# Optimization experiments

Hardware: AMD Instinct MI355X
Metric: run time of the kernel (lower is better)

Reference implementation:

```python
import jax, jax.numpy as jnp
import numpy as np

N, K, CIN, COUT = 150000, 27, 32, 64
EPS = 1e-5
NEG_SLOPE = 0.01


def setup_inputs() -> dict:
    key = jax.random.key(0)
    k1, k2, k3, k4, k5, k6 = jax.random.split(key, 6)
    feats = jax.random.normal(k1, (N, CIN), dtype=jnp.float32)
    nbr = jax.random.randint(k2, (N, K), 0, N, dtype=jnp.int32)
    mask = jax.random.randint(k3, (N, K), 0, 2, dtype=jnp.int32).astype(jnp.bool_)
    # per-offset conv weights [K, Cin, Cout], kaiming-ish scale
    W = jax.random.normal(k4, (K, CIN, COUT), dtype=jnp.float32) / np.sqrt(K * CIN)
    gamma = jax.random.normal(k5, (COUT,), dtype=jnp.float32) * 0.1 + 1.0
    beta = jax.random.normal(k6, (COUT,), dtype=jnp.float32) * 0.1
    return {"feats": feats, "W": W, "gamma": gamma, "beta": beta, "nbr": nbr, "mask": mask}


def reference(feats, W, gamma, beta, nbr, mask):
    # sparse conv as gather-GEMM-(implicit scatter): out[n] = sum_k W[k]^T f[nbr[n,k]]
    gathered = jnp.where(mask[..., None], feats[nbr], 0.0)          # [N, K, Cin]
    out = jnp.einsum('nkc,kcd->nd', gathered, W)                     # [N, Cout]
    # BatchNorm over voxel axis (training-mode batch stats)
    mean = jnp.mean(out, axis=0)
    var = jnp.var(out, axis=0)
    out = (out - mean) * jax.lax.rsqrt(var + EPS) * gamma + beta
    # LeakyReLU, negative_slope = 0.01
    return jnp.where(out >= 0, out, NEG_SLOPE * out)
```

## Files before the change

### kernel.cpp

```cpp
#include <hip/hip_runtime.h>

#define N_VOX  150000
#define KNBR   27
#define CIN    32
#define COUT   64
#define NBUCKET 64
#define NEG_SLOPE 0.01f
#define EPS 1e-5f
#define APPLY_BLOCKS 1024

typedef __bf16 bf16x8 __attribute__((ext_vector_type(8)));
typedef float  f32x4  __attribute__((ext_vector_type(4)));

#define NB_FEATS 2344
#define NB_W       27
#define NB_Z       32

__global__ __launch_bounds__(256) void prep_all(
    const float* __restrict__ feats, const float* __restrict__ W,
    __bf16* __restrict__ fb, __bf16* __restrict__ Wp,
    float* __restrict__ bsums)
{
    const int t = threadIdx.x;
    int b = blockIdx.x;

    if (b < NB_FEATS) {
        const int i = b * 256 + t;
        if (i < N_VOX * CIN / 8) {
            const float4* p = reinterpret_cast<const float4*>(feats) + (size_t)i * 2;
            const float4 a = p[0], c = p[1];
            bf16x8 o;
            o[0]=(__bf16)a.x; o[1]=(__bf16)a.y; o[2]=(__bf16)a.z; o[3]=(__bf16)a.w;
            o[4]=(__bf16)c.x; o[5]=(__bf16)c.y; o[6]=(__bf16)c.z; o[7]=(__bf16)c.w;
            reinterpret_cast<bf16x8*>(fb)[i] = o;
        }
        return;
    }
    b -= NB_FEATS;

    if (b < NB_W) {
        const int u = b * 256 + t;
        const int lane = u & 63, f = u >> 6;
        const int s = f & 3, k = f >> 2;
        const int n = lane & 15, q = lane >> 4;
        const float* src = W + ((size_t)(k * CIN + q * 8) * COUT + s * 16 + n);
        bf16x8 o;
#pragma unroll
        for (int j = 0; j < 8; ++j) o[j] = (__bf16)src[(size_t)j * COUT];
        reinterpret_cast<bf16x8*>(Wp)[u] = o;
        return;
    }
    b -= NB_W;

    const int z = b * 256 + t;
    if (z < NBUCKET * 2 * COUT) bsums[z] = 0.0f;
}

__global__ __launch_bounds__(256, 3) void conv_mfma3(
    const __bf16* __restrict__ fb,
    const __bf16* __restrict__ Wp,
    const int* __restrict__ nbr,
    const int* __restrict__ mask,
    float* __restrict__ out,
    float* __restrict__ bsums)
{
    const int t    = threadIdx.x;
    const int wave = t >> 6;
    const int lane = t & 63;
    const int n16  = lane & 15;
    const int q    = lane >> 4;
    const int arow = blockIdx.x * 64 + wave * 16 + n16;
    const bool rowok = arow < N_VOX;
    const size_t nb = (size_t)(rowok ? arow : 0) * KNBR;

    int idx[KNBR];
#pragma unroll
    for (int k = 0; k < KNBR; ++k) {
        const int m  = mask[nb + k];
        const int ix = nbr[nb + k];
        idx[k] = (rowok && m != 0) ? ix : -1;
    }

    const bf16x8* __restrict__ bp = reinterpret_cast<const bf16x8*>(Wp);
    const bf16x8 zv = {};

    f32x4 acc0 = {0.f,0.f,0.f,0.f}, acc1 = {0.f,0.f,0.f,0.f};
    f32x4 acc2 = {0.f,0.f,0.f,0.f}, acc3 = {0.f,0.f,0.f,0.f};

#pragma unroll 9
    for (int k = 0; k < KNBR; ++k) {
        const bool v  = idx[k] >= 0;
        const int  ie = v ? idx[k] : 0;
        bf16x8 a = *reinterpret_cast<const bf16x8*>(fb + (size_t)ie * CIN + q * 8);
        if (!v) a = zv;
        const bf16x8 b0 = bp[(k * 4 + 0) * 64 + lane];
        const bf16x8 b1 = bp[(k * 4 + 1) * 64 + lane];
        const bf16x8 b2 = bp[(k * 4 + 2) * 64 + lane];
        const bf16x8 b3 = bp[(k * 4 + 3) * 64 + lane];
        acc0 = __builtin_amdgcn_mfma_f32_16x16x32_bf16(a, b0, acc0, 0, 0, 0);
        acc1 = __builtin_amdgcn_mfma_f32_16x16x32_bf16(a, b1, acc1, 0, 0, 0);
        acc2 = __builtin_amdgcn_mfma_f32_16x16x32_bf16(a, b2, acc2, 0, 0, 0);
        acc3 = __builtin_amdgcn_mfma_f32_16x16x32_bf16(a, b3, acc3, 0, 0, 0);
    }

    const int orow_base = blockIdx.x * 64 + wave * 16 + q * 4;
    f32x4 accs[4] = {acc0, acc1, acc2, acc3};
#pragma unroll
    for (int r = 0; r < 4; ++r) {
        const int orow = orow_base + r;
        if (orow < N_VOX) {
            float* dst = out + (size_t)orow * COUT + n16;
#pragma unroll
            for (int s = 0; s < 4; ++s) dst[s * 16] = accs[s][r];
        }
    }

    float* dstb = bsums + ((blockIdx.x * 4 + wave) & (NBUCKET - 1)) * (2 * COUT);
#pragma unroll
    for (int s = 0; s < 4; ++s) {
        float ps = accs[s][0] + accs[s][1] + accs[s][2] + accs[s][3];
        float pq = accs[s][0] * accs[s][0] + accs[s][1] * accs[s][1]
                 + accs[s][2] * accs[s][2] + accs[s][3] * accs[s][3];
        ps += __shfl_down(ps, 32); ps += __shfl_down(ps, 16);
        pq += __shfl_down(pq, 32); pq += __shfl_down(pq, 16);
        if (q == 0) {
            atomicAdd(dstb + s * 16 + n16, ps);
            atomicAdd(dstb + COUT + s * 16 + n16, pq);
        }
    }
}

__global__ __launch_bounds__(256) void bn_stats_apply(
    float* __restrict__ out, const float* __restrict__ bsums,
    const float* __restrict__ gamma, const float* __restrict__ beta)
{
    __shared__ float s_sc[COUT], s_sh[COUT];
    const int t = threadIdx.x;
    if (t < COUT) {
        float s = 0.f, qq = 0.f;
#pragma unroll 8
        for (int b = 0; b < NBUCKET; ++b) {
            s  += bsums[b * (2 * COUT) + t];
            qq += bsums[b * (2 * COUT) + COUT + t];
        }
        const float inv_n = 1.0f / (float)N_VOX;
        const float mean  = s * inv_n;
        const float var   = qq * inv_n - mean * mean;
        const float scale = gamma[t] * rsqrtf(var + EPS);
        s_sc[t] = scale;
        s_sh[t] = beta[t] - mean * scale;
    }
    __syncthreads();

    const long total4 = (long)N_VOX * COUT / 4;
    const long stride = (long)APPLY_BLOCKS * 256;
    long i = (long)blockIdx.x * 256 + t;
    const int cg = (int)(i & 15);
    const float4 sc = reinterpret_cast<const float4*>(s_sc)[cg];
    const float4 sh = reinterpret_cast<const float4*>(s_sh)[cg];
    for (; i < total4; i += stride) {
        float4 v = reinterpret_cast<float4*>(out)[i];
        float x;
        x = fmaf(v.x, sc.x, sh.x); v.x = (x >= 0.f) ? x : NEG_SLOPE * x;
        x = fmaf(v.y, sc.y, sh.y); v.y = (x >= 0.f) ? x : NEG_SLOPE * x;
        x = fmaf(v.z, sc.z, sh.z); v.z = (x >= 0.f) ? x : NEG_SLOPE * x;
        x = fmaf(v.w, sc.w, sh.w); v.w = (x >= 0.f) ? x : NEG_SLOPE * x;
        reinterpret_cast<float4*>(out)[i] = v;
    }
}

#define TM 64
#define FS 68
__global__ __launch_bounds__(256) void conv_f32(
    const float* __restrict__ feats, const float* __restrict__ W,
    const int* __restrict__ nbr, const int* __restrict__ mask,
    float* __restrict__ out, float* __restrict__ bsums)
{
    __shared__ float f_s[CIN * FS];
    __shared__ float w_s[CIN * COUT];
    const int t = threadIdx.x;
    const int tx = t & 15, ty = t >> 4;
    const int base = blockIdx.x * TM;
    const int gr = t >> 2, cq = t & 3;
    const int n_g = base + gr;
    float acc[4][4];
#pragma unroll
    for (int i = 0; i < 4; ++i)
#pragma unroll
        for (int j = 0; j < 4; ++j) acc[i][j] = 0.0f;
    for (int k = 0; k < KNBR; ++k) {
        int idx = -1;
        if (n_g < N_VOX) {
            const long off = (long)n_g * KNBR + k;
            if (mask[off] != 0) idx = nbr[off];
        }
        float4 fa = make_float4(0.f, 0.f, 0.f, 0.f);
        float4 fbv = fa;
        if (idx >= 0) {
            const float4* fp = reinterpret_cast<const float4*>(feats + (long)idx * CIN + cq * 8);
            fa = fp[0]; fbv = fp[1];
        }
        const float4* wsrc = reinterpret_cast<const float4*>(W + (long)k * CIN * COUT + t * 8);
        const float4 wa = wsrc[0], wb = wsrc[1];
        __syncthreads();
        const int c0 = cq * 8;
        f_s[(c0 + 0) * FS + gr] = fa.x; f_s[(c0 + 1) * FS + gr] = fa.y;
        f_s[(c0 + 2) * FS + gr] = fa.z; f_s[(c0 + 3) * FS + gr] = fa.w;
        f_s[(c0 + 4) * FS + gr] = fbv.x; f_s[(c0 + 5) * FS + gr] = fbv.y;
        f_s[(c0 + 6) * FS + gr] = fbv.z; f_s[(c0 + 7) * FS + gr] = fbv.w;
        reinterpret_cast<float4*>(w_s + t * 8)[0] = wa;
        reinterpret_cast<float4*>(w_s + t * 8)[1] = wb;
        __syncthreads();
#pragma unroll
        for (int c = 0; c < CIN; ++c) {
            const float4 fv = *reinterpret_cast<const float4*>(&f_s[c * FS + ty * 4]);
            const float4 wv = *reinterpret_cast<const float4*>(&w_s[c * COUT + tx * 4]);
            const float fr[4] = {fv.x, fv.y, fv.z, fv.w};
            const float wr[4] = {wv.x, wv.y, wv.z, wv.w};
#pragma unroll
            for (int i = 0; i < 4; ++i)
#pragma unroll
                for (int j = 0; j < 4; ++j)
                    acc[i][j] = fmaf(fr[i], wr[j], acc[i][j]);
        }
    }
#pragma unroll
    for (int i = 0; i < 4; ++i) {
        const int n = base + ty * 4 + i;
        if (n < N_VOX)
            *reinterpret_cast<float4*>(out + (long)n * COUT + tx * 4) =
                make_float4(acc[i][0], acc[i][1], acc[i][2], acc[i][3]);
    }
    float psum[4], psq[4];
#pragma unroll
    for (int j = 0; j < 4; ++j) {
        psum[j] = acc[0][j] + acc[1][j] + acc[2][j] + acc[3][j];
        psq[j]  = acc[0][j] * acc[0][j] + acc[1][j] * acc[1][j]
                + acc[2][j] * acc[2][j] + acc[3][j] * acc[3][j];
    }
    __syncthreads();
    *reinterpret_cast<float4*>(&f_s[ty * 64 + tx * 4]) = make_float4(psum[0], psum[1], psum[2], psum[3]);
    *reinterpret_cast<float4*>(&w_s[ty * 64 + tx * 4]) = make_float4(psq[0], psq[1], psq[2], psq[3]);
    __syncthreads();
    if (t < COUT) {
        float s = 0.f, qq = 0.f;
#pragma unroll
        for (int g = 0; g < 16; ++g) { s += f_s[g * 64 + t]; qq += w_s[g * 64 + t]; }
        float* dst = bsums + (blockIdx.x & (NBUCKET - 1)) * (2 * COUT);
        atomicAdd(dst + t, s);
        atomicAdd(dst + COUT + t, qq);
    }
}

extern "C" void kernel_launch(void* const* d_in, const int* in_sizes, int n_in,
                              void* d_out, int out_size, void* d_ws, size_t ws_size,
                              hipStream_t stream) {
    const float* feats = (const float*)d_in[0];
    const float* W     = (const float*)d_in[1];
    const float* gamma = (const float*)d_in[2];
    const float* beta  = (const float*)d_in[3];
    const int* nbr     = (const int*)d_in[4];
    const int* mask    = (const int*)d_in[5];
    float* out = (float*)d_out;
    char* ws   = (char*)d_ws;

    const size_t fb_bytes = (size_t)N_VOX * CIN * sizeof(__bf16);
    const size_t wp_bytes = (size_t)KNBR * 4 * 64 * 8 * sizeof(__bf16);
    const size_t bs_bytes = (size_t)NBUCKET * 2 * COUT * sizeof(float);
    const int conv_blocks = (N_VOX + 63) / 64;

    if (ws_size >= fb_bytes + wp_bytes + bs_bytes) {
        __bf16* fb   = (__bf16*)ws;
        __bf16* Wp   = (__bf16*)(ws + fb_bytes);
        float* bsums = (float*)(ws + fb_bytes + wp_bytes);
        prep_all<<<NB_FEATS + NB_W + NB_Z, 256, 0, stream>>>(feats, W, fb, Wp, bsums);
        conv_mfma3<<<conv_blocks, 256, 0, stream>>>(fb, Wp, nbr, mask, out, bsums);
        bn_stats_apply<<<APPLY_BLOCKS, 256, 0, stream>>>(out, bsums, gamma, beta);
    } else {
        float* bsums = (float*)ws;
        hipMemsetAsync(bsums, 0, bs_bytes, stream);
        conv_f32<<<(N_VOX + TM - 1) / TM, 256, 0, stream>>>(feats, W, nbr, mask, out, bsums);
        bn_stats_apply<<<APPLY_BLOCKS, 256, 0, stream>>>(out, bsums, gamma, beta);
    }
}
```

Before: 179.3 us.

## Process 64 voxels per wave with shared-memory staged neighbor indices

The conv kernel now handles 256 voxels per block (64 per wave, four 16-row MFMA tiles), so each weight fragment loaded per neighbor offset feeds four times as many MFMAs. Neighbor indices and masks are loaded with coalesced reads into shared memory (about 27 KB per block) instead of strided per-thread register loads. The cost is 64 accumulator registers per lane, a lower occupancy target (2 blocks/SM), and fewer, larger blocks, which may reduce latency hiding for the random feature gathers.

```diff
diff --git a/kernel.cpp b/kernel.cpp
--- a/kernel.cpp
+++ b/kernel.cpp
@@ -8,6 +8,7 @@
 #define NEG_SLOPE 0.01f
 #define EPS 1e-5f
 #define APPLY_BLOCKS 1024
+#define VPB 256
 
 typedef __bf16 bf16x8 __attribute__((ext_vector_type(8)));
 typedef float  f32x4  __attribute__((ext_vector_type(4)));
@@ -56,7 +57,7 @@
     if (z < NBUCKET * 2 * COUT) bsums[z] = 0.0f;
 }
 
-__global__ __launch_bounds__(256, 3) void conv_mfma3(
+__global__ __launch_bounds__(256, 2) void conv_mfma4(
     const __bf16* __restrict__ fb,
     const __bf16* __restrict__ Wp,
     const int* __restrict__ nbr,
@@ -64,63 +65,109 @@
     float* __restrict__ out,
     float* __restrict__ bsums)
 {
+    __shared__ int idx_s[VPB * KNBR];
+
     const int t    = threadIdx.x;
+    const int base = blockIdx.x * VPB;
+
+    {
+        const size_t gb  = (size_t)base * KNBR;
+        const int vlim   = N_VOX - base;
+        const int ilim   = (vlim < VPB ? vlim : VPB) * KNBR;
+#pragma unroll
+        for (int j = 0; j < KNBR; ++j) {
+            const int i = t + 256 * j;
+            int v = -1;
+            if (i < ilim) v = (mask[gb + i] != 0) ? nbr[gb + i] : -1;
+            idx_s[i] = v;
+        }
+    }
+    __syncthreads();
+
     const int wave = t >> 6;
     const int lane = t & 63;
     const int n16  = lane & 15;
     const int q    = lane >> 4;
-    const int arow = blockIdx.x * 64 + wave * 16 + n16;
-    const bool rowok = arow < N_VOX;
-    const size_t nb = (size_t)(rowok ? arow : 0) * KNBR;
-
-    int idx[KNBR];
-#pragma unroll
-    for (int k = 0; k < KNBR; ++k) {
-        const int m  = mask[nb + k];
-        const int ix = nbr[nb + k];
-        idx[k] = (rowok && m != 0) ? ix : -1;
-    }
+    const int wb   = wave * 64;
 
     const bf16x8* __restrict__ bp = reinterpret_cast<const bf16x8*>(Wp);
     const bf16x8 zv = {};
 
-    f32x4 acc0 = {0.f,0.f,0.f,0.f}, acc1 = {0.f,0.f,0.f,0.f};
-    f32x4 acc2 = {0.f,0.f,0.f,0.f}, acc3 = {0.f,0.f,0.f,0.f};
-
-#pragma unroll 9
+    const int r0 = (wb +  0 + n16) * KNBR;
+    const int r1 = (wb + 16 + n16) * KNBR;
+    const int r2 = (wb + 32 + n16) * KNBR;
+    const int r3 = (wb + 48 + n16) * KNBR;
+
+    f32x4 acc[4][4];
+#pragma unroll
+    for (int a = 0; a < 4; ++a)
+#pragma unroll
+        for (int b2 = 0; b2 < 4; ++b2) acc[a][b2] = (f32x4){0.f,0.f,0.f,0.f};
+
+#pragma unroll 3
     for (int k = 0; k < KNBR; ++k) {
-        const bool v  = idx[k] >= 0;
-        const int  ie = v ? idx[k] : 0;
-        bf16x8 a = *reinterpret_cast<const bf16x8*>(fb + (size_t)ie * CIN + q * 8);
-        if (!v) a = zv;
+        const int i0 = idx_s[r0 + k];
+        const int i1 = idx_s[r1 + k];
+        const int i2 = idx_s[r2 + k];
+        const int i3 = idx_s[r3 + k];
+
+        bf16x8 a0 = *reinterpret_cast<const bf16x8*>(fb + (size_t)(i0 < 0 ? 0 : i0) * CIN + q * 8);
+        bf16x8 a1 = *reinterpret_cast<const bf16x8*>(fb + (size_t)(i1 < 0 ? 0 : i1) * CIN + q * 8);
+        bf16x8 a2 = *reinterpret_cast<const bf16x8*>(fb + (size_t)(i2 < 0 ? 0 : i2) * CIN + q * 8);
+        bf16x8 a3 = *reinterpret_cast<const bf16x8*>(fb + (size_t)(i3 < 0 ? 0 : i3) * CIN + q * 8);
+        if (i0 < 0) a0 = zv;
+        if (i1 < 0) a1 = zv;
+        if (i2 < 0) a2 = zv;
+        if (i3 < 0) a3 = zv;
+
         const bf16x8 b0 = bp[(k * 4 + 0) * 64 + lane];
         const bf16x8 b1 = bp[(k * 4 + 1) * 64 + lane];
         const bf16x8 b2 = bp[(k * 4 + 2) * 64 + lane];
         const bf16x8 b3 = bp[(k * 4 + 3) * 64 + lane];
-        acc0 = __builtin_amdgcn_mfma_f32_16x16x32_bf16(a, b0, acc0, 0, 0, 0);
-        acc1 = __builtin_amdgcn_mfma_f32_16x16x32_bf16(a, b1, acc1, 0, 0, 0);
-        acc2 = __builtin_amdgcn_mfma_f32_16x16x32_bf16(a, b2, acc2, 0, 0, 0);
-        acc3 = __builtin_amdgcn_mfma_f32_16x16x32_bf16(a, b3, acc3, 0, 0, 0);
-    }
-
-    const int orow_base = blockIdx.x * 64 + wave * 16 + q * 4;
-    f32x4 accs[4] = {acc0, acc1, acc2, acc3};
-#pragma unroll
-    for (int r = 0; r < 4; ++r) {
-        const int orow = orow_base + r;
-        if (orow < N_VOX) {
-            float* dst = out + (size_t)orow * COUT + n16;
-#pragma unroll
-            for (int s = 0; s < 4; ++s) dst[s * 16] = accs[s][r];
+
+        acc[0][0] = __builtin_amdgcn_mfma_f32_16x16x32_bf16(a0, b0, acc[0][0], 0, 0, 0);
+        acc[0][1] = __builtin_amdgcn_mfma_f32_16x16x32_bf16(a0, b1, acc[0][1], 0, 0, 0);
+        acc[0][2] = __builtin_amdgcn_mfma_f32_16x16x32_bf16(a0, b2, acc[0][2], 0, 0, 0);
+        acc[0][3] = __builtin_amdgcn_mfma_f32_16x16x32_bf16(a0, b3, acc[0][3], 0, 0, 0);
+        acc[1][0] = __builtin_amdgcn_mfma_f32_16x16x32_bf16(a1, b0, acc[1][0], 0, 0, 0);
+        acc[1][1] = __builtin_amdgcn_mfma_f32_16x16x32_bf16(a1, b1, acc[1][1], 0, 0, 0);
+        acc[1][2] = __builtin_amdgcn_mfma_f32_16x16x32_bf16(a1, b2, acc[1][2], 0, 0, 0);
+        acc[1][3] = __builtin_amdgcn_mfma_f32_16x16x32_bf16(a1, b3, acc[1][3], 0, 0, 0);
+        acc[2][0] = __builtin_amdgcn_mfma_f32_16x16x32_bf16(a2, b0, acc[2][0], 0, 0, 0);
+        acc[2][1] = __builtin_amdgcn_mfma_f32_16x16x32_bf16(a2, b1, acc[2][1], 0, 0, 0);
+        acc[2][2] = __builtin_amdgcn_mfma_f32_16x16x32_bf16(a2, b2, acc[2][2], 0, 0, 0);
+        acc[2][3] = __builtin_amdgcn_mfma_f32_16x16x32_bf16(a2, b3, acc[2][3], 0, 0, 0);
+        acc[3][0] = __builtin_amdgcn_mfma_f32_16x16x32_bf16(a3, b0, acc[3][0], 0, 0, 0);
+        acc[3][1] = __builtin_amdgcn_mfma_f32_16x16x32_bf16(a3, b1, acc[3][1], 0, 0, 0);
+        acc[3][2] = __builtin_amdgcn_mfma_f32_16x16x32_bf16(a3, b2, acc[3][2], 0, 0, 0);
+        acc[3][3] = __builtin_amdgcn_mfma_f32_16x16x32_bf16(a3, b3, acc[3][3], 0, 0, 0);
+    }
+
+#pragma unroll
+    for (int sl = 0; sl < 4; ++sl) {
+        const int orow_b = base + wb + sl * 16 + q * 4;
+#pragma unroll
+        for (int r = 0; r < 4; ++r) {
+            const int orow = orow_b + r;
+            if (orow < N_VOX) {
+                float* dst = out + (size_t)orow * COUT + n16;
+#pragma unroll
+                for (int s = 0; s < 4; ++s) dst[s * 16] = acc[sl][s][r];
+            }
         }
     }
 
     float* dstb = bsums + ((blockIdx.x * 4 + wave) & (NBUCKET - 1)) * (2 * COUT);
 #pragma unroll
     for (int s = 0; s < 4; ++s) {
-        float ps = accs[s][0] + accs[s][1] + accs[s][2] + accs[s][3];
-        float pq = accs[s][0] * accs[s][0] + accs[s][1] * accs[s][1]
-                 + accs[s][2] * accs[s][2] + accs[s][3] * accs[s][3];
+        float ps = 0.f, pq = 0.f;
+#pragma unroll
+        for (int sl = 0; sl < 4; ++sl)
+#pragma unroll
+            for (int r = 0; r < 4; ++r) {
+                const float x = acc[sl][s][r];
+                ps += x; pq += x * x;
+            }
         ps += __shfl_down(ps, 32); ps += __shfl_down(ps, 16);
         pq += __shfl_down(pq, 32); pq += __shfl_down(pq, 16);
         if (q == 0) {
@@ -267,14 +314,13 @@
     const size_t fb_bytes = (size_t)N_VOX * CIN * sizeof(__bf16);
     const size_t wp_bytes = (size_t)KNBR * 4 * 64 * 8 * sizeof(__bf16);
     const size_t bs_bytes = (size_t)NBUCKET * 2 * COUT * sizeof(float);
-    const int conv_blocks = (N_VOX + 63) / 64;
 
     if (ws_size >= fb_bytes + wp_bytes + bs_bytes) {
         __bf16* fb   = (__bf16*)ws;
         __bf16* Wp   = (__bf16*)(ws + fb_bytes);
         float* bsums = (float*)(ws + fb_bytes + wp_bytes);
         prep_all<<<NB_FEATS + NB_W + NB_Z, 256, 0, stream>>>(feats, W, fb, Wp, bsums);
-        conv_mfma3<<<conv_blocks, 256, 0, stream>>>(fb, Wp, nbr, mask, out, bsums);
+        conv_mfma4<<<(N_VOX + VPB - 1) / VPB, 256, 0, stream>>>(fb, Wp, nbr, mask, out, bsums);
         bn_stats_apply<<<APPLY_BLOCKS, 256, 0, stream>>>(out, bsums, gamma, beta);
     } else {
         float* bsums = (float*)ws;
```

Measured after the change: 171.0 us. 4.7% less time.
